# Performance work log

Measured on AMD Instinct MI355X. Metric: run time of the kernel, lower is better.

The kernel has to match this reference:

```python
import jax, jax.numpy as jnp
import numpy as np

N, D, K, H, G = 200000, 256, 128, 4, 1024  # nodes, emb_dim, hidden, heads, graphs


def setup_inputs() -> dict:
    key = jax.random.key(0)
    k0, k1, k2, k3 = jax.random.split(key, 4)
    node_features = jax.random.normal(k0, (N, D), jnp.float32)
    segment_ids = jnp.sort(jax.random.randint(k1, (N,), 0, G)).astype(jnp.int32)
    W1 = jax.random.normal(k2, (H, D, K), jnp.float32) / np.float32(np.sqrt(D))
    b1 = jnp.zeros((H, K), jnp.float32)
    W2 = jax.random.normal(k3, (H, K), jnp.float32) / np.float32(np.sqrt(K))
    b2 = jnp.zeros((H,), jnp.float32)
    return {"node_features": node_features, "segment_ids": segment_ids,
            "num_graphs": G, "W1": W1, "b1": b1, "W2": W2, "b2": b2}


def _segment_softmax(scores, seg, num_segments):
    # scores: [N, H]; numerically-stable softmax within each graph segment, per head
    m = jax.ops.segment_max(scores, seg, num_segments=num_segments)  # [G, H]
    e = jnp.exp(scores - m[seg])
    s = jax.ops.segment_sum(e, seg, num_segments=num_segments)  # [G, H]
    return e / s[seg]


def reference(node_features, segment_ids, num_graphs, W1, b1, W2, b2):
    # Per-head MLP score for all heads at once: [N, H]
    h = jax.nn.relu(jnp.einsum('nd,hdk->nhk', node_features, W1) + b1)
    scores = jnp.einsum('nhk,hk->nh', h, W2) + b2
    # dgl.softmax_nodes per head == segment softmax over graph ids
    attn = _segment_softmax(scores, segment_ids, num_graphs)  # [N, H]
    # combine_type == 'mean': mean_h segment_sum(attn_h * x)
    # == segment_sum(mean_h(attn_h) * x) since the sum is linear in attn.
    avg_attn = attn.mean(axis=1)  # [N]
    weighted = avg_attn[:, None] * node_features  # [N, D]
    return jax.ops.segment_sum(weighted, segment_ids, num_segments=num_graphs)  # [G, D]
```

## Files before the change

### kernel.cpp

```cpp
#include <hip/hip_runtime.h>
#include <hip/hip_bf16.h>

typedef unsigned short u16;
typedef __attribute__((ext_vector_type(8))) __bf16 bf16x8;
typedef __attribute__((ext_vector_type(8))) u16 u16x8;
typedef __attribute__((ext_vector_type(4))) float f32x4;

__device__ __forceinline__ u16 f2bf(float f) {
    unsigned u = __float_as_uint(f);
    u += 0x7fffu + ((u >> 16) & 1u);
    return (u16)(u >> 16);
}

__global__ __launch_bounds__(256) void transpose_w1(const float* __restrict__ W1,
                                                    u16* __restrict__ W1T) {
    __shared__ u16 tile[64][132];
    const int t = threadIdx.x;
    const int h = blockIdx.x >> 2;
    const int dt = blockIdx.x & 3;
#pragma unroll
    for (int j = 0; j < 8; ++j) {
        int idx = j * 256 + t;
        int r = idx >> 5;
        int kq = idx & 31;
        float4 v = *reinterpret_cast<const float4*>(
            W1 + ((size_t)h * 256 + dt * 64 + r) * 128 + kq * 4);
        ushort4 o;
        o.x = f2bf(v.x); o.y = f2bf(v.y); o.z = f2bf(v.z); o.w = f2bf(v.w);
        *reinterpret_cast<ushort4*>(&tile[r][kq * 4]) = o;
    }
    __syncthreads();
#pragma unroll
    for (int j = 0; j < 4; ++j) {
        int idx = j * 256 + t;
        int k = idx >> 3;
        int c8 = idx & 7;
        u16x8 o;
#pragma unroll
        for (int e = 0; e < 8; ++e) o[e] = tile[c8 * 8 + e][k];
        *reinterpret_cast<u16x8*>(W1T + ((size_t)h * 128 + k) * 256 + dt * 64 + c8 * 8) = o;
    }
}

__global__ __launch_bounds__(256, 2) void score_kernel(
        const float* __restrict__ x, const u16* __restrict__ W1T,
        const float* __restrict__ b1, const float* __restrict__ W2,
        const float* __restrict__ b2, float* __restrict__ scores, int N) {
    __shared__ u16 xb[16384];

    const int t = threadIdx.x;
    const int wave = t >> 6;
    const int lane = t & 63;
    const int l15 = lane & 15;
    const int quad = lane >> 4;
    const int n0 = blockIdx.x * 64;

    const u16* aptr = W1T + ((size_t)wave * 128 + l15) * 256 + quad * 8;

    bf16x8 a0[8], a1[8];
#pragma unroll
    for (int j = 0; j < 8; ++j)
        a0[j] = *reinterpret_cast<const bf16x8*>(aptr + j * 4096);

    {
        const int nrow = wave * 16 + (lane >> 2);
        const int koff = (lane & 3) * 8;
        int nn = n0 + nrow; if (nn >= N) nn = N - 1;
        const float* src = x + (size_t)nn * 256 + koff;
        const int l_t = ((lane & 3) << 4) | (lane >> 2);
        const int q   = l_t ^ ((l_t >> 4) << 1);
        u16* dst = xb + (size_t)wave * 512 + q * 8;
        float4 v[16];
#pragma unroll
        for (int i = 0; i < 8; ++i) {
            v[2 * i]     = *reinterpret_cast<const float4*>(src + i * 32);
            v[2 * i + 1] = *reinterpret_cast<const float4*>(src + i * 32 + 4);
        }
#pragma unroll
        for (int i = 0; i < 8; ++i) {
            u16x8 o;
            o[0] = f2bf(v[2*i].x);   o[1] = f2bf(v[2*i].y);
            o[2] = f2bf(v[2*i].z);   o[3] = f2bf(v[2*i].w);
            o[4] = f2bf(v[2*i+1].x); o[5] = f2bf(v[2*i+1].y);
            o[6] = f2bf(v[2*i+1].z); o[7] = f2bf(v[2*i+1].w);
            *reinterpret_cast<u16x8*>(dst + i * 2048) = o;
        }
    }

    const int qr = lane ^ ((lane >> 4) << 1);
    const u16* xrd = xb + qr * 8;

    __syncthreads();

    f32x4 acc[8][4] = {};
#pragma unroll
    for (int ks = 0; ks < 8; ++ks) {
        auto& a  = (ks & 1) ? a1 : a0;
        auto& an = (ks & 1) ? a0 : a1;
        bf16x8 b[4];
#pragma unroll
        for (int nf = 0; nf < 4; ++nf)
            b[nf] = *reinterpret_cast<const bf16x8*>(xrd + (ks * 4 + nf) * 512);
        if (ks < 7) {
#pragma unroll
            for (int j = 0; j < 8; ++j)
                an[j] = *reinterpret_cast<const bf16x8*>(aptr + j * 4096 + (ks + 1) * 32);
        }
#pragma unroll
        for (int fr = 0; fr < 8; ++fr)
#pragma unroll
            for (int nf = 0; nf < 4; ++nf)
                acc[fr][nf] = __builtin_amdgcn_mfma_f32_16x16x32_bf16(
                    a[fr], b[nf], acc[fr][nf], 0, 0, 0);
    }

    const int h = wave;
    float4 b1v[8], w2v[8];
#pragma unroll
    for (int fr = 0; fr < 8; ++fr) {
        int rb = h * 128 + fr * 16 + quad * 4;
        b1v[fr] = *reinterpret_cast<const float4*>(b1 + rb);
        w2v[fr] = *reinterpret_cast<const float4*>(W2 + rb);
    }
    const float b2v = b2[h];
#pragma unroll
    for (int nf = 0; nf < 4; ++nf) {
        float p = 0.f;
#pragma unroll
        for (int fr = 0; fr < 8; ++fr) {
            f32x4 c = acc[fr][nf];
            p += fmaxf(c[0] + b1v[fr].x, 0.f) * w2v[fr].x
               + fmaxf(c[1] + b1v[fr].y, 0.f) * w2v[fr].y
               + fmaxf(c[2] + b1v[fr].z, 0.f) * w2v[fr].z
               + fmaxf(c[3] + b1v[fr].w, 0.f) * w2v[fr].w;
        }
        p += __shfl_xor(p, 16, 64);
        p += __shfl_xor(p, 32, 64);
        int n = n0 + nf * 16 + lane;
        if (lane < 16 && n < N)
            scores[(size_t)n * 4 + h] = p + b2v;
    }
}

__device__ __forceinline__ int lower_bound(const int* __restrict__ a, int n, int v) {
    int lo = 0, hi = n;
    while (lo < hi) {
        int mid = (lo + hi) >> 1;
        if (a[mid] < v) lo = mid + 1; else hi = mid;
    }
    return lo;
}

__global__ __launch_bounds__(256) void segstat_kernel(
        const float4* __restrict__ scores4, const int* __restrict__ seg,
        float4* __restrict__ mOut, float4* __restrict__ isOut, int N) {
    __shared__ float4 redm[4];
    __shared__ float4 reds[4];
    const int g = blockIdx.x;
    const int t = threadIdx.x;
    const int start = lower_bound(seg, N, g);
    const int end = lower_bound(seg, N, g + 1);

    float4 mx = make_float4(-3.4e38f, -3.4e38f, -3.4e38f, -3.4e38f);
    for (int i = start + t; i < end; i += 256) {
        float4 s = scores4[i];
        mx.x = fmaxf(mx.x, s.x); mx.y = fmaxf(mx.y, s.y);
        mx.z = fmaxf(mx.z, s.z); mx.w = fmaxf(mx.w, s.w);
    }
#pragma unroll
    for (int off = 1; off < 64; off <<= 1) {
        mx.x = fmaxf(mx.x, __shfl_xor(mx.x, off, 64));
        mx.y = fmaxf(mx.y, __shfl_xor(mx.y, off, 64));
        mx.z = fmaxf(mx.z, __shfl_xor(mx.z, off, 64));
        mx.w = fmaxf(mx.w, __shfl_xor(mx.w, off, 64));
    }
    if ((t & 63) == 0) redm[t >> 6] = mx;
    __syncthreads();
    mx = redm[0];
#pragma unroll
    for (int w = 1; w < 4; ++w) {
        mx.x = fmaxf(mx.x, redm[w].x); mx.y = fmaxf(mx.y, redm[w].y);
        mx.z = fmaxf(mx.z, redm[w].z); mx.w = fmaxf(mx.w, redm[w].w);
    }

    float4 sm = make_float4(0.f, 0.f, 0.f, 0.f);
    for (int i = start + t; i < end; i += 256) {
        float4 s = scores4[i];
        sm.x += expf(s.x - mx.x); sm.y += expf(s.y - mx.y);
        sm.z += expf(s.z - mx.z); sm.w += expf(s.w - mx.w);
    }
#pragma unroll
    for (int off = 1; off < 64; off <<= 1) {
        sm.x += __shfl_xor(sm.x, off, 64);
        sm.y += __shfl_xor(sm.y, off, 64);
        sm.z += __shfl_xor(sm.z, off, 64);
        sm.w += __shfl_xor(sm.w, off, 64);
    }
    if ((t & 63) == 0) reds[t >> 6] = sm;
    __syncthreads();
    if (t == 0) {
        float4 tot = reds[0];
        for (int w = 1; w < 4; ++w) {
            tot.x += reds[w].x; tot.y += reds[w].y;
            tot.z += reds[w].z; tot.w += reds[w].w;
        }
        bool nonempty = end > start;
        float4 m_out = nonempty ? mx : make_float4(0.f, 0.f, 0.f, 0.f);
        float4 is;
        is.x = (nonempty && tot.x > 0.f) ? 1.f / tot.x : 0.f;
        is.y = (nonempty && tot.y > 0.f) ? 1.f / tot.y : 0.f;
        is.z = (nonempty && tot.z > 0.f) ? 1.f / tot.z : 0.f;
        is.w = (nonempty && tot.w > 0.f) ? 1.f / tot.w : 0.f;
        mOut[g] = m_out;
        isOut[g] = is;
    }
}

__global__ __launch_bounds__(256) void wsum_kernel(
        const float* __restrict__ x, const float4* __restrict__ scores4,
        const int* __restrict__ seg, const float4* __restrict__ mArr,
        const float4* __restrict__ isArr, float* __restrict__ out, int N) {
    __shared__ float wl[64];
    __shared__ int gl[64];
    __shared__ unsigned long long bmask_s;
    const int t = threadIdx.x;
    const int n0 = blockIdx.x * 64;
    const int cnt = min(64, N - n0);

    if (t < 64) {
        int g = -1;
        float w = 0.f;
        bool bnd = false;
        if (t < cnt) {
            int n = n0 + t;
            g = seg[n];
            float4 s = scores4[n];
            float4 m = mArr[g];
            float4 is = isArr[g];
            w = 0.25f * (expf(s.x - m.x) * is.x + expf(s.y - m.y) * is.y +
                         expf(s.z - m.z) * is.z + expf(s.w - m.w) * is.w);
            bnd = (t > 0) && (g != seg[n - 1]);
        }
        wl[t] = w;
        gl[t] = g;
        unsigned long long bm = __ballot(bnd);
        if (t == 0) bmask_s = bm;
    }
    __syncthreads();
    const unsigned long long bmask = bmask_s;

    int rs = 0;
    while (rs < cnt) {
        unsigned long long mm = (rs < 63) ? (bmask & ((~0ULL) << (rs + 1))) : 0ULL;
        int re = mm ? (__ffsll((long long)mm) - 1) : cnt;
        if (re > cnt) re = cnt;
        float acc = 0.f;
        int i = rs;
        for (; i + 8 <= re; i += 8) {
            float xv[8];
#pragma unroll
            for (int j = 0; j < 8; ++j)
                xv[j] = x[(size_t)(n0 + i + j) * 256 + t];
#pragma unroll
            for (int j = 0; j < 8; ++j) acc += wl[i + j] * xv[j];
        }
        for (; i < re; ++i) acc += wl[i] * x[(size_t)(n0 + i) * 256 + t];
        atomicAdd(&out[(size_t)gl[rs] * 256 + t], acc);
        rs = re;
    }
}

extern "C" void kernel_launch(void* const* d_in, const int* in_sizes, int n_in,
                              void* d_out, int out_size, void* d_ws, size_t ws_size,
                              hipStream_t stream) {
    const float* x  = (const float*)d_in[0];
    const int* seg  = (const int*)d_in[1];
    const float* W1 = (const float*)d_in[3];
    const float* b1 = (const float*)d_in[4];
    const float* W2 = (const float*)d_in[5];
    const float* b2 = (const float*)d_in[6];
    float* out = (float*)d_out;

    const int N = in_sizes[0] / 256;
    const int G = 1024;

    char* ws = (char*)d_ws;
    float* scores = (float*)ws;
    u16* W1T      = (u16*)(ws + (size_t)N * 16);
    float* mArr   = (float*)(ws + (size_t)N * 16 + 262144);
    float* isArr  = mArr + (size_t)G * 4;

    hipMemsetAsync(d_out, 0, (size_t)G * 256 * sizeof(float), stream);
    transpose_w1<<<16, 256, 0, stream>>>(W1, W1T);
    score_kernel<<<(N + 63) / 64, 256, 0, stream>>>(x, W1T, b1, W2, b2, scores, N);
    segstat_kernel<<<G, 256, 0, stream>>>((const float4*)scores, seg,
                                          (float4*)mArr, (float4*)isArr, N);
    wsum_kernel<<<(N + 63) / 64, 256, 0, stream>>>(x, (const float4*)scores, seg,
                                                   (const float4*)mArr,
                                                   (const float4*)isArr, out, N);
}
```

Measured before the change: 436.5 us.

## Stage W1 tiles via LDS and fuse segment stats with per-graph pooling

Measured after the change: 408.6 us. 1.07x faster.

```diff
diff --git a/kernel.cpp b/kernel.cpp
--- a/kernel.cpp
+++ b/kernel.cpp
@@ -10,6 +10,12 @@
     unsigned u = __float_as_uint(f);
     u += 0x7fffu + ((u >> 16) & 1u);
     return (u16)(u >> 16);
+}
+
+__device__ __forceinline__ void gl_lds16(const void* g, void* l) {
+    __builtin_amdgcn_global_load_lds(
+        (const __attribute__((address_space(1))) void*)g,
+        (__attribute__((address_space(3))) void*)l, 16, 0, 0);
 }
 
 __global__ __launch_bounds__(256) void transpose_w1(const float* __restrict__ W1,
@@ -47,6 +53,7 @@
         const float* __restrict__ b1, const float* __restrict__ W2,
         const float* __restrict__ b2, float* __restrict__ scores, int N) {
     __shared__ u16 xb[16384];
+    __shared__ u16 sA[16384];
 
     const int t = threadIdx.x;
     const int wave = t >> 6;
@@ -55,12 +62,15 @@
     const int quad = lane >> 4;
     const int n0 = blockIdx.x * 64;
 
-    const u16* aptr = W1T + ((size_t)wave * 128 + l15) * 256 + quad * 8;
-
-    bf16x8 a0[8], a1[8];
-#pragma unroll
-    for (int j = 0; j < 8; ++j)
-        a0[j] = *reinterpret_cast<const bf16x8*>(aptr + j * 4096);
+    const u16* asrc = W1T + ((size_t)wave * 128 + l15) * 256 + quad * 8;
+
+    auto stageA = [&](int ks) {
+#pragma unroll
+        for (int j = 0; j < 8; ++j)
+            gl_lds16(asrc + j * 4096 + ks * 32, &sA[(size_t)(wave * 8 + j) * 512]);
+    };
+
+    stageA(0);
 
     {
         const int nrow = wave * 16 + (lane >> 2);
@@ -89,29 +99,28 @@
 
     const int qr = lane ^ ((lane >> 4) << 1);
     const u16* xrd = xb + qr * 8;
+    const u16* abase = &sA[(size_t)wave * 4096 + lane * 8];
 
     __syncthreads();
 
     f32x4 acc[8][4] = {};
-#pragma unroll
     for (int ks = 0; ks < 8; ++ks) {
-        auto& a  = (ks & 1) ? a1 : a0;
-        auto& an = (ks & 1) ? a0 : a1;
-        bf16x8 b[4];
+        bf16x8 a[8], b[4];
+#pragma unroll
+        for (int j = 0; j < 8; ++j)
+            a[j] = *reinterpret_cast<const bf16x8*>(abase + j * 512);
 #pragma unroll
         for (int nf = 0; nf < 4; ++nf)
             b[nf] = *reinterpret_cast<const bf16x8*>(xrd + (ks * 4 + nf) * 512);
-        if (ks < 7) {
-#pragma unroll
-            for (int j = 0; j < 8; ++j)
-                an[j] = *reinterpret_cast<const bf16x8*>(aptr + j * 4096 + (ks + 1) * 32);
-        }
+        __syncthreads();
+        if (ks < 7) stageA(ks + 1);
 #pragma unroll
         for (int fr = 0; fr < 8; ++fr)
 #pragma unroll
             for (int nf = 0; nf < 4; ++nf)
                 acc[fr][nf] = __builtin_amdgcn_mfma_f32_16x16x32_bf16(
                     a[fr], b[nf], acc[fr][nf], 0, 0, 0);
+        __syncthreads();
     }
 
     const int h = wave;
@@ -151,15 +160,30 @@
     return lo;
 }
 
-__global__ __launch_bounds__(256) void segstat_kernel(
-        const float4* __restrict__ scores4, const int* __restrict__ seg,
-        float4* __restrict__ mOut, float4* __restrict__ isOut, int N) {
-    __shared__ float4 redm[4];
-    __shared__ float4 reds[4];
+__global__ __launch_bounds__(256) void starts_kernel(
+        const int* __restrict__ seg, int* __restrict__ starts, int N, int G) {
+    int g = blockIdx.x * 256 + threadIdx.x;
+    if (g > G) return;
+    if (g == 0)      starts[0] = 0;
+    else if (g == G) starts[G] = N;
+    else             starts[g] = lower_bound(seg, N, g);
+}
+
+__global__ __launch_bounds__(256) void pool_kernel(
+        const float* __restrict__ x, const float4* __restrict__ scores4,
+        const int* __restrict__ starts, float* __restrict__ out) {
+    __shared__ float4 red[4];
+    __shared__ float wl[256];
     const int g = blockIdx.x;
     const int t = threadIdx.x;
-    const int start = lower_bound(seg, N, g);
-    const int end = lower_bound(seg, N, g + 1);
+    const int lane = t & 63;
+    const int wv = t >> 6;
+    const int start = starts[g];
+    const int end = starts[g + 1];
+    const int len = end - start;
+
+    float* og = out + (size_t)g * 256;
+    if (len == 0) { og[t] = 0.f; return; }
 
     float4 mx = make_float4(-3.4e38f, -3.4e38f, -3.4e38f, -3.4e38f);
     for (int i = start + t; i < end; i += 256) {
@@ -174,14 +198,16 @@
         mx.z = fmaxf(mx.z, __shfl_xor(mx.z, off, 64));
         mx.w = fmaxf(mx.w, __shfl_xor(mx.w, off, 64));
     }
-    if ((t & 63) == 0) redm[t >> 6] = mx;
-    __syncthreads();
-    mx = redm[0];
-#pragma unroll
-    for (int w = 1; w < 4; ++w) {
-        mx.x = fmaxf(mx.x, redm[w].x); mx.y = fmaxf(mx.y, redm[w].y);
-        mx.z = fmaxf(mx.z, redm[w].z); mx.w = fmaxf(mx.w, redm[w].w);
-    }
+    if (lane == 0) red[wv] = mx;
+    __syncthreads();
+    {
+        float4 r0 = red[0], r1 = red[1], r2 = red[2], r3 = red[3];
+        mx.x = fmaxf(fmaxf(r0.x, r1.x), fmaxf(r2.x, r3.x));
+        mx.y = fmaxf(fmaxf(r0.y, r1.y), fmaxf(r2.y, r3.y));
+        mx.z = fmaxf(fmaxf(r0.z, r1.z), fmaxf(r2.z, r3.z));
+        mx.w = fmaxf(fmaxf(r0.w, r1.w), fmaxf(r2.w, r3.w));
+    }
+    __syncthreads();
 
     float4 sm = make_float4(0.f, 0.f, 0.f, 0.f);
     for (int i = start + t; i < end; i += 256) {
@@ -196,78 +222,41 @@
         sm.z += __shfl_xor(sm.z, off, 64);
         sm.w += __shfl_xor(sm.w, off, 64);
     }
-    if ((t & 63) == 0) reds[t >> 6] = sm;
-    __syncthreads();
-    if (t == 0) {
-        float4 tot = reds[0];
-        for (int w = 1; w < 4; ++w) {
-            tot.x += reds[w].x; tot.y += reds[w].y;
-            tot.z += reds[w].z; tot.w += reds[w].w;
-        }
-        bool nonempty = end > start;
-        float4 m_out = nonempty ? mx : make_float4(0.f, 0.f, 0.f, 0.f);
-        float4 is;
-        is.x = (nonempty && tot.x > 0.f) ? 1.f / tot.x : 0.f;
-        is.y = (nonempty && tot.y > 0.f) ? 1.f / tot.y : 0.f;
-        is.z = (nonempty && tot.z > 0.f) ? 1.f / tot.z : 0.f;
-        is.w = (nonempty && tot.w > 0.f) ? 1.f / tot.w : 0.f;
-        mOut[g] = m_out;
-        isOut[g] = is;
-    }
-}
-
-__global__ __launch_bounds__(256) void wsum_kernel(
-        const float* __restrict__ x, const float4* __restrict__ scores4,
-        const int* __restrict__ seg, const float4* __restrict__ mArr,
-        const float4* __restrict__ isArr, float* __restrict__ out, int N) {
-    __shared__ float wl[64];
-    __shared__ int gl[64];
-    __shared__ unsigned long long bmask_s;
-    const int t = threadIdx.x;
-    const int n0 = blockIdx.x * 64;
-    const int cnt = min(64, N - n0);
-
-    if (t < 64) {
-        int g = -1;
+    if (lane == 0) red[wv] = sm;
+    __syncthreads();
+    float4 inv;
+    {
+        float4 r0 = red[0], r1 = red[1], r2 = red[2], r3 = red[3];
+        inv.x = 1.f / (r0.x + r1.x + r2.x + r3.x);
+        inv.y = 1.f / (r0.y + r1.y + r2.y + r3.y);
+        inv.z = 1.f / (r0.z + r1.z + r2.z + r3.z);
+        inv.w = 1.f / (r0.w + r1.w + r2.w + r3.w);
+    }
+
+    float acc = 0.f;
+    for (int c = 0; c < len; c += 256) {
         float w = 0.f;
-        bool bnd = false;
-        if (t < cnt) {
-            int n = n0 + t;
-            g = seg[n];
-            float4 s = scores4[n];
-            float4 m = mArr[g];
-            float4 is = isArr[g];
-            w = 0.25f * (expf(s.x - m.x) * is.x + expf(s.y - m.y) * is.y +
-                         expf(s.z - m.z) * is.z + expf(s.w - m.w) * is.w);
-            bnd = (t > 0) && (g != seg[n - 1]);
-        }
+        if (c + t < len) {
+            float4 s = scores4[start + c + t];
+            w = 0.25f * (expf(s.x - mx.x) * inv.x + expf(s.y - mx.y) * inv.y +
+                         expf(s.z - mx.z) * inv.z + expf(s.w - mx.w) * inv.w);
+        }
+        __syncthreads();
         wl[t] = w;
-        gl[t] = g;
-        unsigned long long bm = __ballot(bnd);
-        if (t == 0) bmask_s = bm;
-    }
-    __syncthreads();
-    const unsigned long long bmask = bmask_s;
-
-    int rs = 0;
-    while (rs < cnt) {
-        unsigned long long mm = (rs < 63) ? (bmask & ((~0ULL) << (rs + 1))) : 0ULL;
-        int re = mm ? (__ffsll((long long)mm) - 1) : cnt;
-        if (re > cnt) re = cnt;
-        float acc = 0.f;
-        int i = rs;
-        for (; i + 8 <= re; i += 8) {
+        __syncthreads();
+        const int cl = min(256, len - c);
+        const float* xp = x + (size_t)(start + c) * 256 + t;
+        int j = 0;
+        for (; j + 8 <= cl; j += 8) {
             float xv[8];
 #pragma unroll
-            for (int j = 0; j < 8; ++j)
-                xv[j] = x[(size_t)(n0 + i + j) * 256 + t];
-#pragma unroll
-            for (int j = 0; j < 8; ++j) acc += wl[i + j] * xv[j];
-        }
-        for (; i < re; ++i) acc += wl[i] * x[(size_t)(n0 + i) * 256 + t];
-        atomicAdd(&out[(size_t)gl[rs] * 256 + t], acc);
-        rs = re;
-    }
+            for (int jj = 0; jj < 8; ++jj) xv[jj] = xp[(size_t)(j + jj) * 256];
+#pragma unroll
+            for (int jj = 0; jj < 8; ++jj) acc += wl[j + jj] * xv[jj];
+        }
+        for (; j < cl; ++j) acc += wl[j] * xp[(size_t)j * 256];
+    }
+    og[t] = acc;
 }
 
 extern "C" void kernel_launch(void* const* d_in, const int* in_sizes, int n_in,
@@ -287,15 +276,10 @@
     char* ws = (char*)d_ws;
     float* scores = (float*)ws;
     u16* W1T      = (u16*)(ws + (size_t)N * 16);
-    float* mArr   = (float*)(ws + (size_t)N * 16 + 262144);
-    float* isArr  = mArr + (size_t)G * 4;
-
-    hipMemsetAsync(d_out, 0, (size_t)G * 256 * sizeof(float), stream);
+    int* starts   = (int*)(ws + (size_t)N * 16 + 262144);
+
     transpose_w1<<<16, 256, 0, stream>>>(W1, W1T);
+    starts_kernel<<<(G + 256) / 256, 256, 0, stream>>>(seg, starts, N, G);
     score_kernel<<<(N + 63) / 64, 256, 0, stream>>>(x, W1T, b1, W2, b2, scores, N);
-    segstat_kernel<<<G, 256, 0, stream>>>((const float4*)scores, seg,
-                                          (float4*)mArr, (float4*)isArr, N);
-    wsum_kernel<<<(N + 63) / 64, 256, 0, stream>>>(x, (const float4*)scores, seg,
-                                                   (const float4*)mArr,
-                                                   (const float4*)isArr, out, N);
-}
+    pool_kernel<<<G, 256, 0, stream>>>(x, (const float4*)scores, starts, out);
+}
```
